# Performance work log

Hardware: AMD Instinct MI355X
Metric: run time of the kernel (lower is better)

Reference implementation:

```python
import jax, jax.numpy as jnp
import numpy as np
from math import log2, floor

B, N, DIM = 2, 2048, 2048
HEADS, DIM_HEAD, FF_MULT = 16, 128, 4
RMS_EPS = 1e-8


def _get_slopes(heads):
    def pow2_slopes(n):
        start = 2 ** (-2 ** (-(log2(n) - 3)))
        return [start * start ** i for i in range(n)]
    if log2(heads).is_integer():
        return pow2_slopes(heads)
    closest = 2 ** floor(log2(heads))
    return pow2_slopes(closest) + pow2_slopes(2 * closest)[0::2][: heads - closest]


def setup_inputs() -> dict:
    key = jax.random.key(0)
    ks = jax.random.split(key, 5)
    std = 0.02
    return {
        "x": jax.random.normal(ks[0], (B, N, DIM), dtype=jnp.float32),
        "g": jnp.ones((DIM,), dtype=jnp.float32),
        "w_qkv": jax.random.normal(ks[1], (DIM, DIM + DIM_HEAD), dtype=jnp.float32) * std,
        "w_attn_out": jax.random.normal(ks[2], (DIM, DIM), dtype=jnp.float32) * std,
        "w_ff1": jax.random.normal(ks[3], (DIM, 2 * FF_MULT * DIM), dtype=jnp.float32) * std,
        "w_ff2": jax.random.normal(ks[4], (FF_MULT * DIM, DIM), dtype=jnp.float32) * std,
    }


def reference(x, g, w_qkv, w_attn_out, w_ff1, w_ff2):
    b, n, dim = x.shape
    # RMSNorm: x / clamp(||x|| * dim^-0.5, eps) * g
    norm = jnp.linalg.norm(x, axis=-1, keepdims=True) * (dim ** -0.5)
    xn = x / jnp.maximum(norm, RMS_EPS) * g

    # Parallel SwiGLU FFN branch (shares normed input with attention)
    h = xn @ w_ff1                       # [b, n, 2*ff_mult*dim]
    val, gate = jnp.split(h, 2, axis=-1)
    ff_out = (jax.nn.silu(gate) * val) @ w_ff2  # [b, n, dim]

    # Multi-query attention: single dim_head-wide kv shared as K and V
    qkv = xn @ w_qkv                     # [b, n, dim + dim_head]
    q, kv = qkv[..., :dim], qkv[..., dim:]
    q = q.reshape(b, n, HEADS, DIM_HEAD) * (DIM_HEAD ** -0.5)
    sim = jnp.einsum('bihd,bjd->bhij', q, kv)  # [b, h, n, n]

    # ALiBi bias: -|j - i| * slope_h
    slopes = jnp.asarray(_get_slopes(HEADS), dtype=sim.dtype)[:, None, None]
    pos = jnp.arange(n)
    bias = -jnp.abs(pos[None, None, :] - pos[None, :, None]).astype(sim.dtype) * slopes
    sim = sim + bias

    # Causal mask (strict upper triangle masked)
    causal = jnp.triu(jnp.ones((n, n), dtype=bool), 1)
    neg = jnp.asarray(jnp.finfo(sim.dtype).max, sim.dtype)
    sim = jnp.where(causal, -neg, sim)

    attn = jax.nn.softmax(sim, axis=-1)
    out = jnp.einsum('bhij,bjd->bhid', attn, kv)     # [b, h, n, dim_head]
    out = out.transpose(0, 2, 1, 3).reshape(b, n, dim)
    return out @ w_attn_out + ff_out
```

## Files before the change

kernel.cpp:

```cpp
#include <hip/hip_runtime.h>
#include <stdint.h>

typedef unsigned short u16;
typedef __attribute__((ext_vector_type(8))) short bf16x8;
typedef __attribute__((ext_vector_type(4))) float f32x4;
typedef __attribute__((ext_vector_type(8))) unsigned short us8;
typedef __attribute__((ext_vector_type(4))) float fvec4;

#define BATCH 2
#define SEQ   2048
#define DIMM  2048
#define NH    16
#define DH    128
#define ROWS  (BATCH*SEQ)
#define QKVN  (DIMM + DH)
#define FFH   8192
#define LOG2E 1.44269504088896340736f

static __device__ __forceinline__ u16 f2bf(float x) {
  union { float f; uint32_t u; } v; v.f = x;
  uint32_t r = (v.u + 0x7fffu + ((v.u >> 16) & 1u)) >> 16;
  return (u16)r;
}

static __device__ __forceinline__ float fast_exp2(float x) {
  float r; asm("v_exp_f32 %0, %1" : "=v"(r) : "v"(x)); return r;
}

static __device__ __forceinline__ void gld_lds16(const void* g, void* l) {
  __builtin_amdgcn_global_load_lds(
      (const __attribute__((address_space(1))) uint32_t*)g,
      (__attribute__((address_space(3))) uint32_t*)l, 16, 0, 0);
}

__global__ __launch_bounds__(256)
void rmsnorm_k(const float* __restrict__ x, const float* __restrict__ g, u16* __restrict__ xn) {
  const int row = blockIdx.x;
  const float* xr = x + (size_t)row * DIMM;
  const int off = threadIdx.x * 8;
  fvec4 a = *(const fvec4*)(xr + off);
  fvec4 b = *(const fvec4*)(xr + off + 4);
  float ss = a[0]*a[0]+a[1]*a[1]+a[2]*a[2]+a[3]*a[3]
           + b[0]*b[0]+b[1]*b[1]+b[2]*b[2]+b[3]*b[3];
  #pragma unroll
  for (int m = 32; m >= 1; m >>= 1) ss += __shfl_xor(ss, m);
  __shared__ float red[4];
  if ((threadIdx.x & 63) == 0) red[threadIdx.x >> 6] = ss;
  __syncthreads();
  float tot = red[0] + red[1] + red[2] + red[3];
  float inv = 1.0f / fmaxf(sqrtf(tot * (1.0f / DIMM)), 1e-8f);
  fvec4 ga = *(const fvec4*)(g + off);
  fvec4 gb = *(const fvec4*)(g + off + 4);
  us8 o;
  #pragma unroll
  for (int i = 0; i < 4; i++) { o[i] = f2bf(a[i]*inv*ga[i]); o[4+i] = f2bf(b[i]*inv*gb[i]); }
  *(us8*)(xn + (size_t)row * DIMM + off) = o;
}

template<typename TIN>
__global__ __launch_bounds__(256)
void transpose_to_bf16(const TIN* __restrict__ in, u16* __restrict__ out, int R, int C) {
  __shared__ u16 tile[64 * 65];
  const int r0 = blockIdx.y * 64, c0 = blockIdx.x * 64;
  const int tr = threadIdx.x >> 2;
  const int tc = (threadIdx.x & 3) * 16;
  const TIN* ip = in + (size_t)(r0 + tr) * C + c0 + tc;
  u16 tmp[16];
  #pragma unroll
  for (int i = 0; i < 16; i++) {
    if constexpr (sizeof(TIN) == 4) tmp[i] = f2bf(((const float*)ip)[i]);
    else                            tmp[i] = ((const u16*)ip)[i];
  }
  #pragma unroll
  for (int i = 0; i < 16; i++) tile[tr * 65 + tc + i] = tmp[i];
  __syncthreads();
  const int oc  = c0 + tr;
  const int orr = (threadIdx.x & 3) * 16;
  us8 v0, v1;
  #pragma unroll
  for (int i = 0; i < 8; i++) v0[i] = tile[(orr + i) * 65 + tr];
  #pragma unroll
  for (int i = 0; i < 8; i++) v1[i] = tile[(orr + 8 + i) * 65 + tr];
  u16* op = out + (size_t)oc * R + r0 + orr;
  *(us8*)op = v0;
  *(us8*)(op + 8) = v1;
}

template<int MODE>
__global__ __launch_bounds__(256, 2)
void gemm_bf16(const u16* __restrict__ A, const u16* __restrict__ BT, int K,
               float* __restrict__ outF, u16* __restrict__ outQ, u16* __restrict__ outKV,
               const float* __restrict__ tmpF) {
  __shared__ __align__(16) u16 lA[128 * 32];
  __shared__ __align__(16) u16 lB[128 * 32];
  const int tid = threadIdx.x;
  const int wave = tid >> 6, lane = tid & 63;
  const int lid = lane & 15, quad = lane >> 4;
  const int wm = wave >> 1, wn = wave & 1;
  const int row0 = blockIdx.y * 128;
  const int col0 = blockIdx.x * 128;
  f32x4 acc[4][4];
  #pragma unroll
  for (int i = 0; i < 4; i++)
    #pragma unroll
    for (int j = 0; j < 4; j++) { acc[i][j][0]=0.f; acc[i][j][1]=0.f; acc[i][j][2]=0.f; acc[i][j][3]=0.f; }

  const int rA0 = wave * 32;
  const int rsub = lane >> 2;
  const int cl = lane & 3;

  for (int k0 = 0; k0 < K; k0 += 32) {
    #pragma unroll
    for (int h2 = 0; h2 < 2; ++h2) {
      int rloc = rA0 + h2 * 16 + rsub;
      int gc = cl ^ ((rloc >> 1) & 3);
      gld_lds16(A  + (size_t)(row0 + rloc) * K + k0 + gc * 8, lA + (rA0 + h2 * 16) * 32);
      gld_lds16(BT + (size_t)(col0 + rloc) * K + k0 + gc * 8, lB + (rA0 + h2 * 16) * 32);
    }
    __syncthreads();
    bf16x8 af[4], bfr[4];
    #pragma unroll
    for (int i = 0; i < 4; i++) {
      int r  = wm * 64 + i * 16 + lid;
      af[i]  = *(const bf16x8*)(lA + r * 32 + (quad ^ ((r >> 1) & 3)) * 8);
      int rb = wn * 64 + i * 16 + lid;
      bfr[i] = *(const bf16x8*)(lB + rb * 32 + (quad ^ ((rb >> 1) & 3)) * 8);
    }
    #pragma unroll
    for (int im = 0; im < 4; im++)
      #pragma unroll
      for (int in = 0; in < 4; in++)
        acc[im][in] = __builtin_amdgcn_mfma_f32_16x16x32_bf16(af[im], bfr[in], acc[im][in], 0, 0, 0);
    __syncthreads();
  }

  #pragma unroll
  for (int im = 0; im < 4; im++)
    #pragma unroll
    for (int in = 0; in < 4; in++) {
      int col = col0 + wn * 64 + in * 16 + lid;
      int rbase = row0 + wm * 64 + im * 16 + quad * 4;
      #pragma unroll
      for (int rg = 0; rg < 4; rg++) {
        float v = acc[im][in][rg];
        int row = rbase + rg;
        if constexpr (MODE == 0) {
          if (col < DIMM) outQ[(size_t)row * DIMM + col] = f2bf(v);
          else            outKV[(size_t)row * DH + (col - DIMM)] = f2bf(v);
        } else if constexpr (MODE == 2) {
          outF[(size_t)row * DIMM + col] = v;
        } else {
          size_t idx = (size_t)row * DIMM + col;
          outF[idx] += v + tmpF[idx];
        }
      }
    }
}

static __device__ __forceinline__ void stage_half(const u16* __restrict__ src, u16* dst,
                                                  int K, int sr, int sgc, int wave) {
  gld_lds16(src + (size_t)sr * K + sgc,       dst + wave * 1024);
  gld_lds16(src + (size_t)(sr + 8) * K + sgc, dst + wave * 1024 + 512);
}

static __device__ __forceinline__ void lda4(bf16x8 (&dst)[4][2], const u16* sAb,
                                            int mh, int wm, int lid, int c0) {
  #pragma unroll
  for (int i = 0; i < 4; ++i) {
    const u16* p = sAb + (mh * 128 + wm * 64 + i * 16 + lid) * 64;
    dst[i][0] = *(const bf16x8*)(p + c0);
    dst[i][1] = *(const bf16x8*)(p + (c0 ^ 32));
  }
}

static __device__ __forceinline__ void ldb2(bf16x8 (&dst)[2][2], const u16* sBb,
                                            int nh, int wn, int lid, int c0) {
  #pragma unroll
  for (int n = 0; n < 2; ++n) {
    const u16* p = sBb + (nh * 128 + wn * 32 + n * 16 + lid) * 64;
    dst[n][0] = *(const bf16x8*)(p + c0);
    dst[n][1] = *(const bf16x8*)(p + (c0 ^ 32));
  }
}

static __device__ __forceinline__ void quad16(f32x4 (&acc)[8][4], const bf16x8 (&af)[4][2],
                                              const bf16x8 (&bf)[2][2], int mh, int nh) {
  __builtin_amdgcn_s_setprio(1);
  #pragma unroll
  for (int i = 0; i < 4; ++i)
    #pragma unroll
    for (int n = 0; n < 2; ++n) {
      f32x4 c = acc[mh * 4 + i][nh * 2 + n];
      c = __builtin_amdgcn_mfma_f32_16x16x32_bf16(af[i][0], bf[n][0], c, 0, 0, 0);
      c = __builtin_amdgcn_mfma_f32_16x16x32_bf16(af[i][1], bf[n][1], c, 0, 0, 0);
      acc[mh * 4 + i][nh * 2 + n] = c;
    }
  __builtin_amdgcn_s_setprio(0);
}

#define VMW(n) asm volatile("s_waitcnt vmcnt(" #n ")" ::: "memory")
#define BAR8() __builtin_amdgcn_s_barrier()

#define EIGHT_PHASE_LOOP(NITER)                                               \
  {                                                                           \
    STAGE_A(0,0,0); STAGE_B(0,0,0); STAGE_B(0,1,0); STAGE_A(0,1,0);           \
    STAGE_A(1,0,1); STAGE_B(1,0,1); STAGE_B(1,1,1);                           \
    VMW(10);                                                                  \
    BAR8();                                                                   \
    for (int I = 0; I < (NITER); ++I) {                                       \
      const bool more = (I + 1 < (NITER));                                    \
      const int kt1 = 2*I+1, kt2 = 2*I+2, kt3 = 2*I+3;                        \
      bf16x8 af[4][2], b0f[2][2], b1f[2][2];                                  \
                                                                      \
      lda4(af, sA[0], 0, wm, lid, c0); ldb2(b0f, sB[0], 0, wn, lid, c0);      \
      STAGE_A(1,1,kt1);                                                       \
      BAR8();                                                                 \
      quad16(acc, af, b0f, 0, 0);                                             \
      if (more) { VMW(10); } else { VMW(0); }                                 \
      BAR8();                                                                 \
                                                                      \
      ldb2(b1f, sB[0], 1, wn, lid, c0);                                       \
      if (more) STAGE_A(0,0,kt2);                                             \
      BAR8();                                                                 \
      quad16(acc, af, b1f, 0, 1);                                             \
      if (more) { VMW(10); }                                                  \
      BAR8();                                                                 \
                                                                      \
      lda4(af, sA[0], 1, wm, lid, c0);                                        \
      if (more) STAGE_B(0,0,kt2);                                             \
      BAR8();                                                                 \
      quad16(acc, af, b1f, 1, 1);                                             \
      BAR8();                                                                 \
                                                                      \
      if (more) STAGE_B(0,1,kt2);                                             \
      BAR8();                                                                 \
      quad16(acc, af, b0f, 1, 0);                                             \
      if (more) { VMW(10); }                                                  \
      BAR8();                                                                 \
                                                                      \
      lda4(af, sA[1], 0, wm, lid, c0); ldb2(b0f, sB[1], 0, wn, lid, c0);      \
      if (more) STAGE_A(0,1,kt2);                                             \
      BAR8();                                                                 \
      quad16(acc, af, b0f, 0, 0);                                             \
      if (more) { VMW(10); }                                                  \
      BAR8();                                                                 \
                                                                      \
      ldb2(b1f, sB[1], 1, wn, lid, c0);                                       \
      if (more) STAGE_A(1,0,kt3);                                             \
      BAR8();                                                                 \
      quad16(acc, af, b1f, 0, 1);                                             \
      if (more) { VMW(10); }                                                  \
      BAR8();                                                                 \
                                                                      \
      lda4(af, sA[1], 1, wm, lid, c0);                                        \
      if (more) STAGE_B(1,0,kt3);                                             \
      BAR8();                                                                 \
      quad16(acc, af, b1f, 1, 1);                                             \
      BAR8();                                                                 \
                                                                      \
      if (more) STAGE_B(1,1,kt3);                                             \
      BAR8();                                                                 \
      quad16(acc, af, b0f, 1, 0);                                             \
      if (more) { VMW(10); }                                                  \
      BAR8();                                                                 \
    }                                                                         \
  }

__global__ __launch_bounds__(512, 2)
void gemm_ff1_swiglu_8p(const u16* __restrict__ A, const u16* __restrict__ BT,
                        u16* __restrict__ FF) {
  __shared__ __align__(16) u16 sA[2][256 * 64];
  __shared__ __align__(16) u16 sB[2][256 * 64];
  const int tid = threadIdx.x;
  const int wave = tid >> 6, lane = tid & 63;
  const int lid = lane & 15, quad = lane >> 4;
  const int wm = wave >> 2, wn = wave & 3;
  const int K = DIMM;

  int orig = blockIdx.y * 64 + blockIdx.x;
  int swz = (orig & 7) * 128 + (orig >> 3);
  const int row0 = (swz >> 6) * 256;
  const int n0 = (swz & 63) * 128;

  const int sr  = wave * 16 + (lane >> 3);
  const int sgc = (((lane & 7) ^ (lane >> 3)) << 3);
  const int c0  = ((quad ^ (lid & 7)) << 3);

  f32x4 acc[8][4];
  #pragma unroll
  for (int i = 0; i < 8; ++i)
    #pragma unroll
    for (int j = 0; j < 4; ++j) { acc[i][j][0]=0.f; acc[i][j][1]=0.f; acc[i][j][2]=0.f; acc[i][j][3]=0.f; }

  #define STAGE_A(b, h, kt) stage_half(A  + (size_t)(row0 + (h)*128) * K + (kt)*64, &sA[b][(h)*8192], K, sr, sgc, wave)
  #define STAGE_B(b, h, kt) stage_half(BT + (size_t)((h) ? (FFH + n0) : n0) * K + (kt)*64, &sB[b][(h)*8192], K, sr, sgc, wave)

  EIGHT_PHASE_LOOP(K / 128)

  #undef STAGE_A
  #undef STAGE_B

  #pragma unroll
  for (int mi = 0; mi < 8; ++mi) {
    const int row = row0 + (mi >> 2) * 128 + wm * 64 + (mi & 3) * 16 + quad * 4;
    #pragma unroll
    for (int n = 0; n < 2; ++n) {
      const int col = n0 + wn * 32 + n * 16 + lid;
      #pragma unroll
      for (int rg = 0; rg < 4; ++rg) {
        float vv = acc[mi][n][rg];
        float gg = acc[mi][2 + n][rg];
        float sig = 1.0f / (1.0f + fast_exp2(-gg * LOG2E));
        FF[(size_t)(row + rg) * FFH + col] = f2bf(vv * gg * sig);
      }
    }
  }
}

__global__ __launch_bounds__(512, 2)
void gemm_ff2_8p(const u16* __restrict__ A, const u16* __restrict__ BT,
                 float* __restrict__ out0, float* __restrict__ out1) {
  __shared__ __align__(16) u16 sA[2][256 * 64];
  __shared__ __align__(16) u16 sB[2][256 * 64];
  const int tid = threadIdx.x;
  const int wave = tid >> 6, lane = tid & 63;
  const int lid = lane & 15, quad = lane >> 4;
  const int wm = wave >> 2, wn = wave & 3;
  const int K = FFH;

  int orig = (blockIdx.z * 16 + blockIdx.y) * 8 + blockIdx.x;
  int swz = (orig & 7) * 32 + (orig >> 3);
  const int n0   = (swz & 7) * 256;
  const int ks   = (swz >> 3) & 1;
  const int row0 = (swz >> 4) * 256;

  const u16* Ab = A  + ks * 4096;
  const u16* Bb = BT + ks * 4096;

  const int sr  = wave * 16 + (lane >> 3);
  const int sgc = (((lane & 7) ^ (lane >> 3)) << 3);
  const int c0  = ((quad ^ (lid & 7)) << 3);

  f32x4 acc[8][4];
  #pragma unroll
  for (int i = 0; i < 8; ++i)
    #pragma unroll
    for (int j = 0; j < 4; ++j) { acc[i][j][0]=0.f; acc[i][j][1]=0.f; acc[i][j][2]=0.f; acc[i][j][3]=0.f; }

  #define STAGE_A(b, h, kt) stage_half(Ab + (size_t)(row0 + (h)*128) * K + (kt)*64, &sA[b][(h)*8192], K, sr, sgc, wave)
  #define STAGE_B(b, h, kt) stage_half(Bb + (size_t)(n0 + (h)*128) * K + (kt)*64,  &sB[b][(h)*8192], K, sr, sgc, wave)

  EIGHT_PHASE_LOOP(32)

  #undef STAGE_A
  #undef STAGE_B

  float* dst = ks ? out1 : out0;
  #pragma unroll
  for (int mi = 0; mi < 8; ++mi) {
    const int row = row0 + (mi >> 2) * 128 + wm * 64 + (mi & 3) * 16 + quad * 4;
    #pragma unroll
    for (int j = 0; j < 4; ++j) {
      const int col = n0 + (j >> 1) * 128 + wn * 32 + (j & 1) * 16 + lid;
      #pragma unroll
      for (int rg = 0; rg < 4; ++rg)
        dst[(size_t)(row + rg) * DIMM + col] = acc[mi][j][rg];
    }
  }
}

__global__ __launch_bounds__(256, 1)
void attn_k2(const u16* __restrict__ qws, const u16* __restrict__ kvws,
             const u16* __restrict__ kvt, u16* __restrict__ attnws) {
  __shared__ __align__(16) u16 kvls[128 * 128];
  __shared__ __align__(16) u16 kvtls[128 * 128];
  __shared__ __align__(16) u16 plds[4][32][136];
  const int tid = threadIdx.x;
  const int wave = tid >> 6, lane = tid & 63;
  const int lid = lane & 15, quad = lane >> 4;
  const int hb = blockIdx.y;
  const int h = hb & (NH - 1), b = hb >> 4;
  const int pair = blockIdx.x;
  const float slope2 = fast_exp2(-0.5f * (float)(h + 1)) * LOG2E;
  const float scale2 = 0.08838834764831845f * LOG2E;
  const float NEG = -__builtin_inff();

  const u16* kvb  = kvws + (size_t)b * SEQ * DH;
  const u16* kvtb = kvt  + (size_t)b * DH * SEQ;

  #pragma unroll 1
  for (int tt = 0; tt < 2; tt++) {
    const int T = tt ? (15 - pair) : pair;
    const int rw = T * 128 + wave * 32;

    bf16x8 qf[2][4];
    #pragma unroll
    for (int ig = 0; ig < 2; ig++)
      #pragma unroll
      for (int ks = 0; ks < 4; ks++)
        qf[ig][ks] = *(const bf16x8*)(qws + (size_t)(b * SEQ + rw + ig * 16 + lid) * DIMM
                                       + h * DH + ks * 32 + quad * 8);
    float srow2[2][4];
    #pragma unroll
    for (int ig = 0; ig < 2; ig++)
      #pragma unroll
      for (int rg = 0; rg < 4; rg++)
        srow2[ig][rg] = slope2 * (float)(rw + ig * 16 + quad * 4 + rg);

    f32x4 o[2][8];
    #pragma unroll
    for (int ig = 0; ig < 2; ig++)
      #pragma unroll
      for (int nd = 0; nd < 8; nd++) { o[ig][nd][0]=0.f; o[ig][nd][1]=0.f; o[ig][nd][2]=0.f; o[ig][nd][3]=0.f; }
    float m2[2][4], l[2][4];
    #pragma unroll
    for (int ig = 0; ig < 2; ig++)
      #pragma unroll
      for (int rg = 0; rg < 4; rg++) { m2[ig][rg] = NEG; l[ig][rg] = 0.f; }

    const int njt = T + 1;
    #pragma unroll 1
    for (int jt = 0; jt < njt; jt++) {
      const int j0 = jt * 128;
      __syncthreads();
      {
        const int c = lane & 15;
        const int r4 = lane >> 4;
        #pragma unroll
        for (int it = 0; it < 8; it++) {
          const int r = wave * 32 + it * 4 + r4;
          const int gc = c ^ (r & 15);
          gld_lds16(kvb  + (size_t)(j0 + r) * DH + gc * 8,        kvls  + (wave * 32 + it * 4) * 128);
          gld_lds16(kvtb + (size_t)r * SEQ + j0 + gc * 8,         kvtls + (wave * 32 + it * 4) * 128);
        }
      }
      __syncthreads();

      const int rhi = rw + 31;
      const int nbmax = min(8, ((rhi - j0) >> 4) + 1);
      const int ks2max = (nbmax + 1) >> 1;

      float pvv[2][8][4];
      float mt[2][4];
      #pragma unroll
      for (int ig = 0; ig < 2; ig++)
        #pragma unroll
        for (int rg = 0; rg < 4; rg++) mt[ig][rg] = NEG;

      #pragma unroll
      for (int nb = 0; nb < 8; nb++) {
        if (nb < nbmax) {
          bf16x8 bk[4];
          #pragma unroll
          for (int ks = 0; ks < 4; ks++)
            bk[ks] = *(const bf16x8*)(kvls + (nb * 16 + lid) * 128 + (((ks * 4 + quad) ^ lid) << 3));
          f32x4 s0, s1;
          s0[0]=0.f;s0[1]=0.f;s0[2]=0.f;s0[3]=0.f;
          s1[0]=0.f;s1[1]=0.f;s1[2]=0.f;s1[3]=0.f;
          #pragma unroll
          for (int ks = 0; ks < 4; ks++) {
            s0 = __builtin_amdgcn_mfma_f32_16x16x32_bf16(qf[0][ks], bk[ks], s0, 0, 0, 0);
            s1 = __builtin_amdgcn_mfma_f32_16x16x32_bf16(qf[1][ks], bk[ks], s1, 0, 0, 0);
          }
          const int jl = j0 + nb * 16 + lid;
          const float sj = slope2 * (float)jl;
          #pragma unroll
          for (int rg = 0; rg < 4; rg++) {
            const int row0r = rw + quad * 4 + rg;
            float e0 = fmaf(s0[rg], scale2, sj) - srow2[0][rg];
            e0 = (jl <= row0r) ? e0 : NEG;
            pvv[0][nb][rg] = e0;
            mt[0][rg] = fmaxf(mt[0][rg], e0);
            float e1 = fmaf(s1[rg], scale2, sj) - srow2[1][rg];
            e1 = (jl <= row0r + 16) ? e1 : NEG;
            pvv[1][nb][rg] = e1;
            mt[1][rg] = fmaxf(mt[1][rg], e1);
          }
        }
      }

      float alpha[2][4];
      #pragma unroll
      for (int ig = 0; ig < 2; ig++)
        #pragma unroll
        for (int rg = 0; rg < 4; rg++) {
          float m = mt[ig][rg];
          m = fmaxf(m, __shfl_xor(m, 1));
          m = fmaxf(m, __shfl_xor(m, 2));
          m = fmaxf(m, __shfl_xor(m, 4));
          m = fmaxf(m, __shfl_xor(m, 8));
          float mn = fmaxf(m2[ig][rg], m);
          alpha[ig][rg] = fast_exp2(m2[ig][rg] - mn);
          m2[ig][rg] = mn;
        }

      float rs[2][4];
      #pragma unroll
      for (int ig = 0; ig < 2; ig++)
        #pragma unroll
        for (int rg = 0; rg < 4; rg++) rs[ig][rg] = 0.f;
      #pragma unroll
      for (int nb = 0; nb < 8; nb++) {
        if (nb < nbmax) {
          #pragma unroll
          for (int ig = 0; ig < 2; ig++)
            #pragma unroll
            for (int rg = 0; rg < 4; rg++) {
              float p = fast_exp2(pvv[ig][nb][rg] - m2[ig][rg]);
              rs[ig][rg] += p;
              plds[wave][ig * 16 + quad * 4 + rg][nb * 16 + lid] = f2bf(p);
            }
        }
      }
      if (nbmax & 1) {
        #pragma unroll
        for (int ig = 0; ig < 2; ig++)
          #pragma unroll
          for (int rg = 0; rg < 4; rg++)
            plds[wave][ig * 16 + quad * 4 + rg][nbmax * 16 + lid] = 0;
      }

      #pragma unroll
      for (int ig = 0; ig < 2; ig++)
        #pragma unroll
        for (int rg = 0; rg < 4; rg++) {
          float r = rs[ig][rg];
          r += __shfl_xor(r, 1);
          r += __shfl_xor(r, 2);
          r += __shfl_xor(r, 4);
          r += __shfl_xor(r, 8);
          l[ig][rg] = l[ig][rg] * alpha[ig][rg] + r;
        }
      #pragma unroll
      for (int ig = 0; ig < 2; ig++)
        #pragma unroll
        for (int nd = 0; nd < 8; nd++)
          #pragma unroll
          for (int rg = 0; rg < 4; rg++) o[ig][nd][rg] *= alpha[ig][rg];

      asm volatile("s_waitcnt lgkmcnt(0)" ::: "memory");
      #pragma unroll
      for (int ks2 = 0; ks2 < 4; ks2++) {
        if (ks2 < ks2max) {
          bf16x8 pa0 = *(const bf16x8*)&plds[wave][lid][ks2 * 32 + quad * 8];
          bf16x8 pa1 = *(const bf16x8*)&plds[wave][16 + lid][ks2 * 32 + quad * 8];
          #pragma unroll
          for (int nd = 0; nd < 8; nd++) {
            bf16x8 bv = *(const bf16x8*)(kvtls + (nd * 16 + lid) * 128 + (((ks2 * 4 + quad) ^ lid) << 3));
            o[0][nd] = __builtin_amdgcn_mfma_f32_16x16x32_bf16(pa0, bv, o[0][nd], 0, 0, 0);
            o[1][nd] = __builtin_amdgcn_mfma_f32_16x16x32_bf16(pa1, bv, o[1][nd], 0, 0, 0);
          }
        }
      }
    }

    #pragma unroll
    for (int ig = 0; ig < 2; ig++) {
      float inv[4];
      #pragma unroll
      for (int rg = 0; rg < 4; rg++) inv[rg] = 1.0f / l[ig][rg];
      #pragma unroll
      for (int nd = 0; nd < 8; nd++)
        #pragma unroll
        for (int rg = 0; rg < 4; rg++) {
          int row = rw + ig * 16 + quad * 4 + rg;
          attnws[(size_t)(b * SEQ + row) * DIMM + h * DH + nd * 16 + lid] =
              f2bf(o[ig][nd][rg] * inv[rg]);
        }
    }
  }
}

extern "C" void kernel_launch(void* const* d_in, const int* in_sizes, int n_in,
                              void* d_out, int out_size, void* d_ws, size_t ws_size,
                              hipStream_t stream) {
  (void)in_sizes; (void)n_in; (void)out_size; (void)ws_size;
  const float* x     = (const float*)d_in[0];
  const float* g     = (const float*)d_in[1];
  const float* w_qkv = (const float*)d_in[2];
  const float* w_ao  = (const float*)d_in[3];
  const float* w_ff1 = (const float*)d_in[4];
  const float* w_ff2 = (const float*)d_in[5];
  float* out = (float*)d_out;

  u16* ws = (u16*)d_ws;
  u16* xn     = ws;
  u16* wTqkv  = xn     + 8388608;
  u16* wTattn = wTqkv  + 4456448;
  u16* wTff1  = wTattn + 4194304;
  u16* wTff2  = wTff1  + 33554432;
  u16* ffin   = wTff2  + 16777216;
  u16* qws    = ffin   + 33554432;
  u16* kvws   = qws    + 8388608;
  u16* kvtws  = kvws   + 524288;
  u16* attnws = kvtws  + 524288;
  float* tmpf = (float*)wTff1;

  transpose_to_bf16<float><<<dim3(QKVN/64, DIMM/64), 256, 0, stream>>>(w_qkv, wTqkv, DIMM, QKVN);
  transpose_to_bf16<float><<<dim3(DIMM/64, DIMM/64), 256, 0, stream>>>(w_ao, wTattn, DIMM, DIMM);
  transpose_to_bf16<float><<<dim3((2*FFH)/64, DIMM/64), 256, 0, stream>>>(w_ff1, wTff1, DIMM, 2*FFH);
  transpose_to_bf16<float><<<dim3(DIMM/64, FFH/64), 256, 0, stream>>>(w_ff2, wTff2, FFH, DIMM);

  rmsnorm_k<<<ROWS, 256, 0, stream>>>(x, g, xn);

  gemm_bf16<0><<<dim3(QKVN/128, ROWS/128), 256, 0, stream>>>(xn, wTqkv, DIMM, nullptr, qws, kvws, nullptr);

  transpose_to_bf16<u16><<<dim3(DH/64, SEQ/64), 256, 0, stream>>>(kvws, kvtws, SEQ, DH);
  transpose_to_bf16<u16><<<dim3(DH/64, SEQ/64), 256, 0, stream>>>(kvws + (size_t)SEQ*DH, kvtws + (size_t)DH*SEQ, SEQ, DH);

  attn_k2<<<dim3(8, NH*BATCH), 256, 0, stream>>>(qws, kvws, kvtws, attnws);

  gemm_ff1_swiglu_8p<<<dim3(FFH/128, ROWS/256), 512, 0, stream>>>(xn, wTff1, ffin);
  gemm_ff2_8p<<<dim3(8, 16, 2), 512, 0, stream>>>(ffin, wTff2, out, tmpf);

  gemm_bf16<3><<<dim3(DIMM/128, ROWS/128), 256, 0, stream>>>(attnws, wTattn, DIMM, out, nullptr, nullptr, tmpf);
}
```

Measured before the change: 966.1 us.

## Overlap LDS fragment loads with MFMA and retune vmcnt waits in eight-phase GEMM loop

Restructures the eight-phase GEMM main loop so that the shared-memory fragment loads for the next phase are issued right after the current MFMA block, before the barrier. The first fragments are preloaded ahead of the loop. The fragment registers are hoisted out of the loop and double-named (bW/bX), and the global-load wait counts are retuned from 10 to 8/6/4/2/0 to match the new staging order. The goal is to hide LDS read latency behind MFMA work and reduce stalls at barriers, at the cost of tighter correctness reasoning about which LDS buffers are still valid when read.

```diff
diff --git a/kernel.cpp b/kernel.cpp
--- a/kernel.cpp
+++ b/kernel.cpp
@@ -205,63 +205,68 @@
   {                                                                           \
     STAGE_A(0,0,0); STAGE_B(0,0,0); STAGE_B(0,1,0); STAGE_A(0,1,0);           \
     STAGE_A(1,0,1); STAGE_B(1,0,1); STAGE_B(1,1,1);                           \
-    VMW(10);                                                                  \
+    VMW(6);                                                                   \
     BAR8();                                                                   \
+    lda4(af, sA[0], 0, wm, lid, c0);                              \
+    ldb2(bW, sB[0], 0, wn, lid, c0);                              \
     for (int I = 0; I < (NITER); ++I) {                                       \
       const bool more = (I + 1 < (NITER));                                    \
       const int kt1 = 2*I+1, kt2 = 2*I+2, kt3 = 2*I+3;                        \
-      bf16x8 af[4][2], b0f[2][2], b1f[2][2];                                  \
-                                                                      \
-      lda4(af, sA[0], 0, wm, lid, c0); ldb2(b0f, sB[0], 0, wn, lid, c0);      \
+                                         \
       STAGE_A(1,1,kt1);                                                       \
       BAR8();                                                                 \
-      quad16(acc, af, b0f, 0, 0);                                             \
-      if (more) { VMW(10); } else { VMW(0); }                                 \
-      BAR8();                                                                 \
-                                                                      \
-      ldb2(b1f, sB[0], 1, wn, lid, c0);                                       \
+      quad16(acc, af, bW, 0, 0);                                              \
+      ldb2(bX, sB[0], 1, wn, lid, c0);                                        \
+      VMW(8);                                                                 \
+      BAR8();                                                                 \
+                                            \
       if (more) STAGE_A(0,0,kt2);                                             \
       BAR8();                                                                 \
-      quad16(acc, af, b1f, 0, 1);                                             \
-      if (more) { VMW(10); }                                                  \
-      BAR8();                                                                 \
-                                                                      \
+      quad16(acc, af, bX, 0, 1);                                              \
       lda4(af, sA[0], 1, wm, lid, c0);                                        \
+      BAR8();                                                                 \
+                                                              \
       if (more) STAGE_B(0,0,kt2);                                             \
       BAR8();                                                                 \
-      quad16(acc, af, b1f, 1, 1);                                             \
-      BAR8();                                                                 \
-                                                                      \
+      quad16(acc, af, bX, 1, 1);                                              \
+      if (more) { VMW(8); } else { VMW(4); }                                  \
+      BAR8();                                                                 \
+                                    \
       if (more) STAGE_B(0,1,kt2);                                             \
       BAR8();                                                                 \
-      quad16(acc, af, b0f, 1, 0);                                             \
-      if (more) { VMW(10); }                                                  \
-      BAR8();                                                                 \
-                                                                      \
-      lda4(af, sA[1], 0, wm, lid, c0); ldb2(b0f, sB[1], 0, wn, lid, c0);      \
+      quad16(acc, af, bW, 1, 0);                                              \
+      ldb2(bW, sB[1], 0, wn, lid, c0);                                        \
+      lda4(af, sA[1], 0, wm, lid, c0);                                        \
+      if (more) { VMW(8); } else { VMW(2); }                                  \
+      BAR8();                                                                 \
+                                         \
       if (more) STAGE_A(0,1,kt2);                                             \
       BAR8();                                                                 \
-      quad16(acc, af, b0f, 0, 0);                                             \
-      if (more) { VMW(10); }                                                  \
-      BAR8();                                                                 \
-                                                                      \
-      ldb2(b1f, sB[1], 1, wn, lid, c0);                                       \
+      quad16(acc, af, bW, 0, 0);                                              \
+      ldb2(bX, sB[1], 1, wn, lid, c0);                                        \
+      if (more) { VMW(8); } else { VMW(0); }                                  \
+      BAR8();                                                                 \
+                                            \
       if (more) STAGE_A(1,0,kt3);                                             \
       BAR8();                                                                 \
-      quad16(acc, af, b1f, 0, 1);                                             \
-      if (more) { VMW(10); }                                                  \
-      BAR8();                                                                 \
-                                                                      \
+      quad16(acc, af, bX, 0, 1);                                              \
       lda4(af, sA[1], 1, wm, lid, c0);                                        \
+      BAR8();                                                                 \
+                                                              \
       if (more) STAGE_B(1,0,kt3);                                             \
       BAR8();                                                                 \
-      quad16(acc, af, b1f, 1, 1);                                             \
-      BAR8();                                                                 \
-                                                                      \
+      quad16(acc, af, bX, 1, 1);                                              \
+      if (more) { VMW(8); }                                                   \
+      BAR8();                                                                 \
+                                  \
       if (more) STAGE_B(1,1,kt3);                                             \
       BAR8();                                                                 \
-      quad16(acc, af, b0f, 1, 0);                                             \
-      if (more) { VMW(10); }                                                  \
+      quad16(acc, af, bW, 1, 0);                                              \
+      if (more) {                                                             \
+        ldb2(bW, sB[0], 0, wn, lid, c0);                                      \
+        lda4(af, sA[0], 0, wm, lid, c0);                                      \
+        VMW(8);                                                               \
+      }                                                                       \
       BAR8();                                                                 \
     }                                                                         \
   }
@@ -291,6 +296,7 @@
   for (int i = 0; i < 8; ++i)
     #pragma unroll
     for (int j = 0; j < 4; ++j) { acc[i][j][0]=0.f; acc[i][j][1]=0.f; acc[i][j][2]=0.f; acc[i][j][3]=0.f; }
+  bf16x8 af[4][2], bW[2][2], bX[2][2];
 
   #define STAGE_A(b, h, kt) stage_half(A  + (size_t)(row0 + (h)*128) * K + (kt)*64, &sA[b][(h)*8192], K, sr, sgc, wave)
   #define STAGE_B(b, h, kt) stage_half(BT + (size_t)((h) ? (FFH + n0) : n0) * K + (kt)*64, &sB[b][(h)*8192], K, sr, sgc, wave)
@@ -346,6 +352,7 @@
   for (int i = 0; i < 8; ++i)
     #pragma unroll
     for (int j = 0; j < 4; ++j) { acc[i][j][0]=0.f; acc[i][j][1]=0.f; acc[i][j][2]=0.f; acc[i][j][3]=0.f; }
+  bf16x8 af[4][2], bW[2][2], bX[2][2];
 
   #define STAGE_A(b, h, kt) stage_half(Ab + (size_t)(row0 + (h)*128) * K + (kt)*64, &sA[b][(h)*8192], K, sr, sgc, wave)
   #define STAGE_B(b, h, kt) stage_half(Bb + (size_t)(n0 + (h)*128) * K + (kt)*64,  &sB[b][(h)*8192], K, sr, sgc, wave)
```

Result: faster. 924.6 us (-4.3%).
